# Kernel tuning notes

Hardware: AMD Instinct MI355X
Metric: run time of the kernel (lower is better)

The kernel has to match this reference:

```python
import jax, jax.numpy as jnp
import numpy as np

N_NODES = 50000
N_EDGES = 800000
N_GRAPHS = 512
IN_CH, HID_CH, OUT_CH, N_CLASSES = 128, 64, 64, 10


def gcn_conv(x, src, dst, ew, W, b, n_nodes):
    """PyG GCNConv: add self-loops (weight 1), symmetric normalization, x @ W, scatter-add at dst, + bias."""
    xw = x @ W  # [N, out]
    loop = jnp.arange(n_nodes, dtype=src.dtype)
    src_f = jnp.concatenate([src, loop])
    dst_f = jnp.concatenate([dst, loop])
    ew_f = jnp.concatenate([ew, jnp.ones((n_nodes,), dtype=ew.dtype)])
    deg = jax.ops.segment_sum(ew_f, dst_f, num_segments=n_nodes)  # [N]
    dinv = jnp.where(deg > 0, jax.lax.rsqrt(deg), 0.0)
    norm = dinv[src_f] * ew_f * dinv[dst_f]  # [E+N]
    msg = norm[:, None] * xw[src_f]  # gather + scale
    out = jax.ops.segment_sum(msg, dst_f, num_segments=n_nodes)  # scatter-add
    return out + b


def setup_inputs() -> dict:
    key = jax.random.key(0)
    ks = jax.random.split(key, 12)
    x = jax.random.normal(ks[0], (N_NODES, IN_CH), dtype=jnp.float32)
    edge_index = jax.random.randint(ks[1], (2, N_EDGES), 0, N_NODES, dtype=jnp.int64)
    edge_attr = jax.random.uniform(ks[2], (N_EDGES,), dtype=jnp.float32)
    batch = jnp.sort(jax.random.randint(ks[3], (N_NODES,), 0, N_GRAPHS, dtype=jnp.int64))
    def glorot(k, shape):
        lim = np.sqrt(6.0 / (shape[0] + shape[1]))
        return jax.random.uniform(k, shape, jnp.float32, -lim, lim)
    W1 = glorot(ks[4], (IN_CH, HID_CH))
    b1 = jnp.zeros((HID_CH,), jnp.float32)
    W2 = glorot(ks[5], (HID_CH, OUT_CH))
    b2 = jnp.zeros((OUT_CH,), jnp.float32)
    LW1 = glorot(ks[6], (OUT_CH, 32))
    Lb1 = jnp.zeros((32,), jnp.float32)
    LW2 = glorot(ks[7], (32, N_CLASSES))
    Lb2 = jnp.zeros((N_CLASSES,), jnp.float32)
    return {"x": x, "edge_index": edge_index, "edge_attr": edge_attr, "batch": batch,
            "W1": W1, "b1": b1, "W2": W2, "b2": b2,
            "LW1": LW1, "Lb1": Lb1, "LW2": LW2, "Lb2": Lb2}


def reference(x, edge_index, edge_attr, batch, W1, b1, W2, b2, LW1, Lb1, LW2, Lb2):
    src, dst = edge_index[0], edge_index[1]
    h = gcn_conv(x, src, dst, edge_attr, W1, b1, N_NODES)
    h = jax.nn.relu(h)
    h = gcn_conv(h, src, dst, edge_attr, W2, b2, N_NODES)
    # global mean pool over graphs
    sums = jax.ops.segment_sum(h, batch, num_segments=N_GRAPHS)  # [G, OUT]
    cnt = jax.ops.segment_sum(jnp.ones((N_NODES,), h.dtype), batch, num_segments=N_GRAPHS)
    pooled = sums / jnp.maximum(cnt, 1.0)[:, None]
    # head (dropout treated as identity for deterministic reference)
    h1 = pooled @ LW1 + Lb1
    return h1 @ LW2 + Lb2
```

## Files before the change

kernel.cpp:

```cpp
#include <hip/hip_runtime.h>
#include <hip/hip_bf16.h>

static constexpr int NN = 50000;
static constexpr int NE = 800000;
static constexpr int NG = 512;
static constexpr int NB = 196;
static constexpr int GEMM_BLOCKS = (NN + 63) / 64;
static constexpr int HB = 128;

__device__ __forceinline__ float bfu(ushort u) {
    return __uint_as_float((unsigned)u << 16);
}
__device__ __forceinline__ ushort fbf(float f) {
    return __hip_bfloat16_raw(__float2bfloat16(f)).x;
}


__global__ void zero_kernel(float* __restrict__ p, int n) {
    int i = blockIdx.x * blockDim.x + threadIdx.x;
    if (i < n) p[i] = 0.f;
}

template <int K, bool BF16IN>
__device__ __forceinline__ void gemm_body(const void* __restrict__ Xv,
                                          const float* __restrict__ W,
                                          ushort* __restrict__ out,
                                          int row0, float Xs[][68], float Ws[][64]) {
    int tx = threadIdx.x & 15, ty = threadIdx.x >> 4;
    float acc[4][4] = {};
    for (int kb = 0; kb < K; kb += 64) {
        __syncthreads();
        for (int i = threadIdx.x; i < 1024; i += 256) {
            int kk = i >> 4, c4 = i & 15;
            *(float4*)&Ws[kk][c4 * 4] = *(const float4*)&W[(kb + kk) * 64 + c4 * 4];
        }
        if constexpr (BF16IN) {
            const ushort* X = (const ushort*)Xv;
            for (int i = threadIdx.x; i < 512; i += 256) {
                int r = i >> 3, g = i & 7;
                int gr = row0 + r; if (gr >= NN) gr = NN - 1;
                uint4 v = *(const uint4*)(X + (long long)gr * K + kb + g * 8);
                float4 f0, f1;
                f0.x = __uint_as_float(v.x << 16); f0.y = __uint_as_float(v.x & 0xffff0000u);
                f0.z = __uint_as_float(v.y << 16); f0.w = __uint_as_float(v.y & 0xffff0000u);
                f1.x = __uint_as_float(v.z << 16); f1.y = __uint_as_float(v.z & 0xffff0000u);
                f1.z = __uint_as_float(v.w << 16); f1.w = __uint_as_float(v.w & 0xffff0000u);
                *(float4*)&Xs[r][g * 8] = f0;
                *(float4*)&Xs[r][g * 8 + 4] = f1;
            }
        } else {
            const float* X = (const float*)Xv;
            for (int i = threadIdx.x; i < 1024; i += 256) {
                int r = i >> 4, k4 = i & 15;
                int gr = row0 + r; if (gr >= NN) gr = NN - 1;
                float4 v = *(const float4*)(X + (long long)gr * K + kb + k4 * 4);
                *(float4*)&Xs[r][k4 * 4] = v;
            }
        }
        __syncthreads();
#pragma unroll
        for (int k4 = 0; k4 < 16; ++k4) {
            float4 w0 = *(const float4*)&Ws[k4 * 4 + 0][tx * 4];
            float4 w1 = *(const float4*)&Ws[k4 * 4 + 1][tx * 4];
            float4 w2 = *(const float4*)&Ws[k4 * 4 + 2][tx * 4];
            float4 w3 = *(const float4*)&Ws[k4 * 4 + 3][tx * 4];
            float4 x0 = *(const float4*)&Xs[ty * 4 + 0][k4 * 4];
            float4 x1 = *(const float4*)&Xs[ty * 4 + 1][k4 * 4];
            float4 x2 = *(const float4*)&Xs[ty * 4 + 2][k4 * 4];
            float4 x3 = *(const float4*)&Xs[ty * 4 + 3][k4 * 4];
#define GCN_ROW(j, xv) \
            acc[j][0]=fmaf(xv.x,w0.x,acc[j][0]); acc[j][1]=fmaf(xv.x,w0.y,acc[j][1]); \
            acc[j][2]=fmaf(xv.x,w0.z,acc[j][2]); acc[j][3]=fmaf(xv.x,w0.w,acc[j][3]); \
            acc[j][0]=fmaf(xv.y,w1.x,acc[j][0]); acc[j][1]=fmaf(xv.y,w1.y,acc[j][1]); \
            acc[j][2]=fmaf(xv.y,w1.z,acc[j][2]); acc[j][3]=fmaf(xv.y,w1.w,acc[j][3]); \
            acc[j][0]=fmaf(xv.z,w2.x,acc[j][0]); acc[j][1]=fmaf(xv.z,w2.y,acc[j][1]); \
            acc[j][2]=fmaf(xv.z,w2.z,acc[j][2]); acc[j][3]=fmaf(xv.z,w2.w,acc[j][3]); \
            acc[j][0]=fmaf(xv.w,w3.x,acc[j][0]); acc[j][1]=fmaf(xv.w,w3.y,acc[j][1]); \
            acc[j][2]=fmaf(xv.w,w3.z,acc[j][2]); acc[j][3]=fmaf(xv.w,w3.w,acc[j][3]);
            GCN_ROW(0, x0)
            GCN_ROW(1, x1)
            GCN_ROW(2, x2)
            GCN_ROW(3, x3)
#undef GCN_ROW
        }
    }
#pragma unroll
    for (int j = 0; j < 4; ++j) {
        int r = row0 + ty * 4 + j;
        if (r < NN) {
            ushort4 sv;
            sv.x = fbf(acc[j][0]); sv.y = fbf(acc[j][1]);
            sv.z = fbf(acc[j][2]); sv.w = fbf(acc[j][3]);
            *(ushort4*)(out + (long long)r * 64 + tx * 4) = sv;
        }
    }
}

__global__ __launch_bounds__(256) void hist_gemm_kernel(const int* __restrict__ dst,
                                                        const float* __restrict__ ew,
                                                        unsigned long long* __restrict__ h,
                                                        int* __restrict__ rank,
                                                        const float* __restrict__ X,
                                                        const float* __restrict__ W,
                                                        ushort* __restrict__ out) {
    __shared__ float Xs[64][68];
    __shared__ float Ws[64][64];
    if (blockIdx.x < HB) {
        for (int e = blockIdx.x * 256 + threadIdx.x; e < NE; e += HB * 256) {
            int d = dst[e];
            unsigned int fx = __float2uint_rn(ew[e] * 1048576.0f);
            unsigned long long pack = (1ULL << 40) | (unsigned long long)fx;
            unsigned long long old = atomicAdd(&h[d], pack);
            rank[e] = (int)(old >> 40);
        }
        return;
    }
    gemm_body<128, false>(X, W, out, (blockIdx.x - HB) * 64, Xs, Ws);
}

template <int K, bool BF16IN>
__global__ __launch_bounds__(256) void gemm_kernel(const void* __restrict__ Xv,
                                                   const float* __restrict__ W,
                                                   ushort* __restrict__ out) {
    __shared__ float Xs[64][68];
    __shared__ float Ws[64][64];
    gemm_body<K, BF16IN>(Xv, W, out, blockIdx.x * 64, Xs, Ws);
}

__global__ __launch_bounds__(256) void dinv_scanA_kernel(const unsigned long long* __restrict__ h,
                                                         float* __restrict__ dinv,
                                                         int* __restrict__ partial) {
    int i = blockIdx.x * 256 + threadIdx.x;
    int cnt = 0;
    if (i < NN) {
        unsigned long long v = h[i];
        cnt = (int)(v >> 40);
        float deg = (float)(v & ((1ULL << 40) - 1)) * (1.0f / 1048576.0f) + 1.0f;
        dinv[i] = 1.0f / sqrtf(deg);
    }
    __shared__ int wsum[4];
    int lane = threadIdx.x & 63, wid = threadIdx.x >> 6;
    int v = cnt;
#pragma unroll
    for (int off = 32; off > 0; off >>= 1) v += __shfl_down(v, (unsigned)off, 64);
    if (lane == 0) wsum[wid] = v;
    __syncthreads();
    if (threadIdx.x == 0) partial[blockIdx.x] = wsum[0] + wsum[1] + wsum[2] + wsum[3];
}

__device__ __forceinline__ int block_scan_inclusive(int v, int* wtot) {
    int lane = threadIdx.x & 63, wid = threadIdx.x >> 6;
    int inc = v;
#pragma unroll
    for (int off = 1; off < 64; off <<= 1) {
        int n = __shfl_up(inc, (unsigned)off, 64);
        if (lane >= off) inc += n;
    }
    if (lane == 63) wtot[wid] = inc;
    __syncthreads();
    int add = 0;
    for (int w = 0; w < wid; ++w) add += wtot[w];
    return inc + add;
}

__global__ __launch_bounds__(256) void scanC_bounds_kernel(const unsigned long long* __restrict__ h,
                                                           const int* __restrict__ partial,
                                                           int* __restrict__ rowptr,
                                                           const int* __restrict__ batch,
                                                           int* __restrict__ gbeg,
                                                           int* __restrict__ gend) {
    __shared__ int wtot[4];
    __shared__ int poff_s;
    int t = threadIdx.x;
    if (t < 64) {
        int s = 0;
        for (int i = t; i < (int)blockIdx.x; i += 64) s += partial[i];
#pragma unroll
        for (int off = 32; off > 0; off >>= 1) s += __shfl_down(s, (unsigned)off, 64);
        if (t == 0) poff_s = s;
    }
    int i = blockIdx.x * 256 + t;
    int v = (i < NN) ? (int)(h[i] >> 40) : 0;
    int incl = block_scan_inclusive(v, wtot);
    if (i < NN) {
        rowptr[i + 1] = poff_s + incl;
        int g = batch[i];
        if (i == 0 || batch[i - 1] != g) gbeg[g] = i;
        if (i == NN - 1 || batch[i + 1] != g) gend[g] = i + 1;
    }
    if (i == 0) rowptr[0] = 0;
}

__global__ __launch_bounds__(256) void scatter_kernel(const int* __restrict__ src,
                                                      const int* __restrict__ dst,
                                                      const float* __restrict__ ew,
                                                      const float* __restrict__ dinv,
                                                      const int* __restrict__ rowptr,
                                                      const int* __restrict__ rank,
                                                      int2* __restrict__ epack) {
    int e = blockIdx.x * blockDim.x + threadIdx.x;
    if (e >= NE) return;
    int s = src[e], d = dst[e];
    int pos = rowptr[d] + rank[e];
    float coef = dinv[s] * ew[e];
    epack[pos] = make_int2(s, __float_as_int(coef));
}

template <bool RELU>
__global__ __launch_bounds__(256) void agg_kernel(const ushort* __restrict__ xw,
                                                  const int* __restrict__ rowptr,
                                                  const int2* __restrict__ epack,
                                                  const float* __restrict__ dinv,
                                                  const float* __restrict__ bias,
                                                  ushort* __restrict__ out) {
    int node = blockIdx.x * 4 + (threadIdx.x >> 6);
    if (node >= NN) return;
    int lane = threadIdx.x & 63;
    int q = lane >> 4;
    int l = lane & 15;
    int beg = rowptr[node], end = rowptr[node + 1];
    float a0 = 0.f, a1 = 0.f, a2 = 0.f, a3 = 0.f;
    float b0 = 0.f, b1 = 0.f, b2 = 0.f, b3 = 0.f;
    int j = beg + q;
    for (; j + 4 < end; j += 8) {
        int2 pA = epack[j];
        int2 pB = epack[j + 4];
        ushort4 uA = *(const ushort4*)(xw + pA.x * 64 + 4 * l);
        ushort4 uB = *(const ushort4*)(xw + pB.x * 64 + 4 * l);
        float wA = __int_as_float(pA.y);
        float wB = __int_as_float(pB.y);
        a0 = fmaf(wA, bfu(uA.x), a0); a1 = fmaf(wA, bfu(uA.y), a1);
        a2 = fmaf(wA, bfu(uA.z), a2); a3 = fmaf(wA, bfu(uA.w), a3);
        b0 = fmaf(wB, bfu(uB.x), b0); b1 = fmaf(wB, bfu(uB.y), b1);
        b2 = fmaf(wB, bfu(uB.z), b2); b3 = fmaf(wB, bfu(uB.w), b3);
    }
    if (j < end) {
        int2 pA = epack[j];
        ushort4 uA = *(const ushort4*)(xw + pA.x * 64 + 4 * l);
        float wA = __int_as_float(pA.y);
        a0 = fmaf(wA, bfu(uA.x), a0); a1 = fmaf(wA, bfu(uA.y), a1);
        a2 = fmaf(wA, bfu(uA.z), a2); a3 = fmaf(wA, bfu(uA.w), a3);
    }
    a0 += b0; a1 += b1; a2 += b2; a3 += b3;
    a0 += __shfl_xor(a0, 16); a0 += __shfl_xor(a0, 32);
    a1 += __shfl_xor(a1, 16); a1 += __shfl_xor(a1, 32);
    a2 += __shfl_xor(a2, 16); a2 += __shfl_xor(a2, 32);
    a3 += __shfl_xor(a3, 16); a3 += __shfl_xor(a3, 32);
    if (q == 0) {
        float di = dinv[node];
        float d2 = di * di;
        ushort4 us = *(const ushort4*)(xw + node * 64 + 4 * l);
        float4 bv = *(const float4*)(bias + 4 * l);
        float o0 = fmaf(di, a0, fmaf(d2, bfu(us.x), bv.x));
        float o1 = fmaf(di, a1, fmaf(d2, bfu(us.y), bv.y));
        float o2 = fmaf(di, a2, fmaf(d2, bfu(us.z), bv.z));
        float o3 = fmaf(di, a3, fmaf(d2, bfu(us.w), bv.w));
        if (RELU) {
            o0 = fmaxf(o0, 0.f); o1 = fmaxf(o1, 0.f);
            o2 = fmaxf(o2, 0.f); o3 = fmaxf(o3, 0.f);
        }
        ushort4 sv;
        sv.x = fbf(o0); sv.y = fbf(o1); sv.z = fbf(o2); sv.w = fbf(o3);
        *(ushort4*)(out + node * 64 + 4 * l) = sv;
    }
}

__global__ __launch_bounds__(256) void poolhead_kernel(const ushort* __restrict__ h,
                                                       const int* __restrict__ gbeg,
                                                       const int* __restrict__ gend,
                                                       const float* __restrict__ LW1,
                                                       const float* __restrict__ Lb1,
                                                       const float* __restrict__ LW2,
                                                       const float* __restrict__ Lb2,
                                                       float* __restrict__ out) {
    __shared__ float pp[4][64];
    __shared__ float p[64];
    __shared__ float t1[32];
    int g = blockIdx.x, t = threadIdx.x;
    int lane = t & 63, wid = t >> 6;
    int b = gbeg[g], e = gend[g];
    float acc = 0.f;
    for (int i = b + wid; i < e; i += 4) acc += bfu(h[i * 64 + lane]);
    pp[wid][lane] = acc;
    __syncthreads();
    if (t < 64) {
        float s = pp[0][t] + pp[1][t] + pp[2][t] + pp[3][t];
        p[t] = s / fmaxf((float)(e - b), 1.0f);
    }
    __syncthreads();
    if (t < 32) {
        float a = Lb1[t];
#pragma unroll
        for (int k = 0; k < 64; ++k) a = fmaf(p[k], LW1[k * 32 + t], a);
        t1[t] = a;
    }
    __syncthreads();
    if (t < 10) {
        float a = Lb2[t];
#pragma unroll
        for (int j = 0; j < 32; ++j) a = fmaf(t1[j], LW2[j * 10 + t], a);
        out[g * 10 + t] = a;
    }
}


extern "C" void kernel_launch(void* const* d_in, const int* in_sizes, int n_in,
                              void* d_out, int out_size, void* d_ws, size_t ws_size,
                              hipStream_t stream) {
    const float* x     = (const float*)d_in[0];
    const int*   ei    = (const int*)d_in[1];
    const float* ew    = (const float*)d_in[2];
    const int*   batch = (const int*)d_in[3];
    const float* W1    = (const float*)d_in[4];
    const float* b1    = (const float*)d_in[5];
    const float* W2    = (const float*)d_in[6];
    const float* b2    = (const float*)d_in[7];
    const float* LW1   = (const float*)d_in[8];
    const float* Lb1   = (const float*)d_in[9];
    const float* LW2   = (const float*)d_in[10];
    const float* Lb2   = (const float*)d_in[11];

    const int* src = ei;
    const int* dst = ei + NE;

    float* ws = (float*)d_ws;
    unsigned long long* h64 = (unsigned long long*)ws;
    int*   gbeg   = (int*)(ws + 100096);
    int*   gend   = (int*)(ws + 100608);
    float* dinv   = ws + 101120;
    int*   rowptr = (int*)(ws + 151168);
    int*   partial= (int*)(ws + 201216);
    int2*  epack  = (int2*)(ws + 201472);
    ushort* xwA   = (ushort*)(ws + 1801472);
    ushort* h12   = (ushort*)(ws + 3401472);
    int*   rank   = (int*)(ws + 5001472);

    zero_kernel<<<(101120 + 255) / 256, 256, 0, stream>>>(ws, 101120);

    hist_gemm_kernel<<<HB + GEMM_BLOCKS, 256, 0, stream>>>(dst, ew, h64, rank, x, W1, xwA);
    dinv_scanA_kernel<<<NB, 256, 0, stream>>>(h64, dinv, partial);
    scanC_bounds_kernel<<<NB, 256, 0, stream>>>(h64, partial, rowptr, batch, gbeg, gend);
    scatter_kernel<<<(NE + 255) / 256, 256, 0, stream>>>(src, dst, ew, dinv, rowptr, rank, epack);

    agg_kernel<true><<<(NN + 3) / 4, 256, 0, stream>>>(xwA, rowptr, epack, dinv, b1, h12);

    gemm_kernel<64, true><<<GEMM_BLOCKS, 256, 0, stream>>>(h12, W2, xwA);
    agg_kernel<false><<<(NN + 3) / 4, 256, 0, stream>>>(xwA, rowptr, epack, dinv, b2, h12);

    poolhead_kernel<<<NG, 256, 0, stream>>>(h12, gbeg, gend, LW1, Lb1, LW2, Lb2, (float*)d_out);
}
```

Baseline: 243.7 us.

## Split degree histogram into two tables, merge scan kernels, widen aggregation loads

The degree/rank histogram now alternates edges between two atomic tables by thread parity to halve contention, with more histogram blocks and two atomics issued per loop iteration; scatter adds the first table's count for odd edges. The two scan passes are merged into one kernel that recomputes block prefix offsets directly from the histograms and also computes dinv, removing a launch. The aggregation kernel now processes 8 edges per wave with 16-byte row loads and 8 accumulators. Costs include zeroing a larger workspace and redundant prefix summation in each scan block.

```diff
diff --git a/kernel.cpp b/kernel.cpp
--- a/kernel.cpp
+++ b/kernel.cpp
@@ -6,7 +6,7 @@
 static constexpr int NG = 512;
 static constexpr int NB = 196;
 static constexpr int GEMM_BLOCKS = (NN + 63) / 64;
-static constexpr int HB = 128;
+static constexpr int HB = 240;
 
 __device__ __forceinline__ float bfu(ushort u) {
     return __uint_as_float((unsigned)u << 16);
@@ -98,7 +98,8 @@
 
 __global__ __launch_bounds__(256) void hist_gemm_kernel(const int* __restrict__ dst,
                                                         const float* __restrict__ ew,
-                                                        unsigned long long* __restrict__ h,
+                                                        unsigned long long* __restrict__ hA,
+                                                        unsigned long long* __restrict__ hB,
                                                         int* __restrict__ rank,
                                                         const float* __restrict__ X,
                                                         const float* __restrict__ W,
@@ -106,12 +107,25 @@
     __shared__ float Xs[64][68];
     __shared__ float Ws[64][64];
     if (blockIdx.x < HB) {
-        for (int e = blockIdx.x * 256 + threadIdx.x; e < NE; e += HB * 256) {
-            int d = dst[e];
-            unsigned int fx = __float2uint_rn(ew[e] * 1048576.0f);
-            unsigned long long pack = (1ULL << 40) | (unsigned long long)fx;
-            unsigned long long old = atomicAdd(&h[d], pack);
-            rank[e] = (int)(old >> 40);
+        const int T = HB * 256;
+        int tid = blockIdx.x * 256 + threadIdx.x;
+        unsigned long long* tab = (tid & 1) ? hB : hA;
+        for (int e = tid; e < NE; e += 2 * T) {
+            int e1 = e + T;
+            bool has1 = e1 < NE;
+            int d0 = dst[e];
+            float v0 = ew[e];
+            int d1 = has1 ? dst[e1] : 0;
+            float v1 = has1 ? ew[e1] : 0.f;
+            unsigned long long p0 = (1ULL << 40) |
+                (unsigned long long)__float2uint_rn(v0 * 1048576.0f);
+            unsigned long long p1 = (1ULL << 40) |
+                (unsigned long long)__float2uint_rn(v1 * 1048576.0f);
+            unsigned long long o0 = atomicAdd(&tab[d0], p0);
+            unsigned long long o1 = 0;
+            if (has1) o1 = atomicAdd(&tab[d1], p1);
+            rank[e] = (int)(o0 >> 40);
+            if (has1) rank[e1] = (int)(o1 >> 40);
         }
         return;
     }
@@ -127,27 +141,6 @@
     gemm_body<K, BF16IN>(Xv, W, out, blockIdx.x * 64, Xs, Ws);
 }
 
-__global__ __launch_bounds__(256) void dinv_scanA_kernel(const unsigned long long* __restrict__ h,
-                                                         float* __restrict__ dinv,
-                                                         int* __restrict__ partial) {
-    int i = blockIdx.x * 256 + threadIdx.x;
-    int cnt = 0;
-    if (i < NN) {
-        unsigned long long v = h[i];
-        cnt = (int)(v >> 40);
-        float deg = (float)(v & ((1ULL << 40) - 1)) * (1.0f / 1048576.0f) + 1.0f;
-        dinv[i] = 1.0f / sqrtf(deg);
-    }
-    __shared__ int wsum[4];
-    int lane = threadIdx.x & 63, wid = threadIdx.x >> 6;
-    int v = cnt;
-#pragma unroll
-    for (int off = 32; off > 0; off >>= 1) v += __shfl_down(v, (unsigned)off, 64);
-    if (lane == 0) wsum[wid] = v;
-    __syncthreads();
-    if (threadIdx.x == 0) partial[blockIdx.x] = wsum[0] + wsum[1] + wsum[2] + wsum[3];
-}
-
 __device__ __forceinline__ int block_scan_inclusive(int v, int* wtot) {
     int lane = threadIdx.x & 63, wid = threadIdx.x >> 6;
     int inc = v;
@@ -163,27 +156,38 @@
     return inc + add;
 }
 
-__global__ __launch_bounds__(256) void scanC_bounds_kernel(const unsigned long long* __restrict__ h,
-                                                           const int* __restrict__ partial,
-                                                           int* __restrict__ rowptr,
-                                                           const int* __restrict__ batch,
-                                                           int* __restrict__ gbeg,
-                                                           int* __restrict__ gend) {
+__global__ __launch_bounds__(256) void scan_kernel(const unsigned long long* __restrict__ hA,
+                                                   const unsigned long long* __restrict__ hB,
+                                                   float* __restrict__ dinv,
+                                                   int* __restrict__ rowptr,
+                                                   const int* __restrict__ batch,
+                                                   int* __restrict__ gbeg,
+                                                   int* __restrict__ gend) {
+    __shared__ int ws4[4];
     __shared__ int wtot[4];
-    __shared__ int poff_s;
     int t = threadIdx.x;
-    if (t < 64) {
-        int s = 0;
-        for (int i = t; i < (int)blockIdx.x; i += 64) s += partial[i];
-#pragma unroll
-        for (int off = 32; off > 0; off >>= 1) s += __shfl_down(s, (unsigned)off, 64);
-        if (t == 0) poff_s = s;
-    }
-    int i = blockIdx.x * 256 + t;
-    int v = (i < NN) ? (int)(h[i] >> 40) : 0;
-    int incl = block_scan_inclusive(v, wtot);
+    int start = blockIdx.x * 256;
+    int s = 0;
+    for (int j = t; j < start; j += 256)
+        s += (int)(hA[j] >> 40) + (int)(hB[j] >> 40);
+    int lane = t & 63, wid = t >> 6;
+#pragma unroll
+    for (int off = 32; off > 0; off >>= 1) s += __shfl_down(s, (unsigned)off, 64);
+    if (lane == 0) ws4[wid] = s;
+    __syncthreads();
+    int poff = ws4[0] + ws4[1] + ws4[2] + ws4[3];
+    int i = start + t;
+    int cnt = 0;
     if (i < NN) {
-        rowptr[i + 1] = poff_s + incl;
+        unsigned long long va = hA[i], vb = hB[i];
+        constexpr unsigned long long M = (1ULL << 40) - 1;
+        cnt = (int)(va >> 40) + (int)(vb >> 40);
+        float deg = (float)((va & M) + (vb & M)) * (1.0f / 1048576.0f) + 1.0f;
+        dinv[i] = 1.0f / sqrtf(deg);
+    }
+    int incl = block_scan_inclusive(cnt, wtot);
+    if (i < NN) {
+        rowptr[i + 1] = poff + incl;
         int g = batch[i];
         if (i == 0 || batch[i - 1] != g) gbeg[g] = i;
         if (i == NN - 1 || batch[i + 1] != g) gend[g] = i + 1;
@@ -197,11 +201,13 @@
                                                       const float* __restrict__ dinv,
                                                       const int* __restrict__ rowptr,
                                                       const int* __restrict__ rank,
+                                                      const unsigned long long* __restrict__ hA,
                                                       int2* __restrict__ epack) {
     int e = blockIdx.x * blockDim.x + threadIdx.x;
     if (e >= NE) return;
     int s = src[e], d = dst[e];
     int pos = rowptr[d] + rank[e];
+    if (e & 1) pos += (int)(hA[d] >> 40);
     float coef = dinv[s] * ew[e];
     epack[pos] = make_int2(s, __float_as_int(coef));
 }
@@ -216,52 +222,51 @@
     int node = blockIdx.x * 4 + (threadIdx.x >> 6);
     if (node >= NN) return;
     int lane = threadIdx.x & 63;
-    int q = lane >> 4;
-    int l = lane & 15;
+    int e8 = lane >> 3;
+    int l8 = lane & 7;
     int beg = rowptr[node], end = rowptr[node + 1];
     float a0 = 0.f, a1 = 0.f, a2 = 0.f, a3 = 0.f;
-    float b0 = 0.f, b1 = 0.f, b2 = 0.f, b3 = 0.f;
-    int j = beg + q;
-    for (; j + 4 < end; j += 8) {
-        int2 pA = epack[j];
-        int2 pB = epack[j + 4];
-        ushort4 uA = *(const ushort4*)(xw + pA.x * 64 + 4 * l);
-        ushort4 uB = *(const ushort4*)(xw + pB.x * 64 + 4 * l);
-        float wA = __int_as_float(pA.y);
-        float wB = __int_as_float(pB.y);
-        a0 = fmaf(wA, bfu(uA.x), a0); a1 = fmaf(wA, bfu(uA.y), a1);
-        a2 = fmaf(wA, bfu(uA.z), a2); a3 = fmaf(wA, bfu(uA.w), a3);
-        b0 = fmaf(wB, bfu(uB.x), b0); b1 = fmaf(wB, bfu(uB.y), b1);
-        b2 = fmaf(wB, bfu(uB.z), b2); b3 = fmaf(wB, bfu(uB.w), b3);
-    }
-    if (j < end) {
-        int2 pA = epack[j];
-        ushort4 uA = *(const ushort4*)(xw + pA.x * 64 + 4 * l);
-        float wA = __int_as_float(pA.y);
-        a0 = fmaf(wA, bfu(uA.x), a0); a1 = fmaf(wA, bfu(uA.y), a1);
-        a2 = fmaf(wA, bfu(uA.z), a2); a3 = fmaf(wA, bfu(uA.w), a3);
-    }
-    a0 += b0; a1 += b1; a2 += b2; a3 += b3;
-    a0 += __shfl_xor(a0, 16); a0 += __shfl_xor(a0, 32);
-    a1 += __shfl_xor(a1, 16); a1 += __shfl_xor(a1, 32);
-    a2 += __shfl_xor(a2, 16); a2 += __shfl_xor(a2, 32);
-    a3 += __shfl_xor(a3, 16); a3 += __shfl_xor(a3, 32);
-    if (q == 0) {
+    float a4 = 0.f, a5 = 0.f, a6 = 0.f, a7 = 0.f;
+    for (int j = beg + e8; j < end; j += 8) {
+        int2 p = epack[j];
+        uint4 v = *(const uint4*)(xw + p.x * 64 + l8 * 8);
+        float w = __int_as_float(p.y);
+        a0 = fmaf(w, __uint_as_float(v.x << 16), a0);
+        a1 = fmaf(w, __uint_as_float(v.x & 0xffff0000u), a1);
+        a2 = fmaf(w, __uint_as_float(v.y << 16), a2);
+        a3 = fmaf(w, __uint_as_float(v.y & 0xffff0000u), a3);
+        a4 = fmaf(w, __uint_as_float(v.z << 16), a4);
+        a5 = fmaf(w, __uint_as_float(v.z & 0xffff0000u), a5);
+        a6 = fmaf(w, __uint_as_float(v.w << 16), a6);
+        a7 = fmaf(w, __uint_as_float(v.w & 0xffff0000u), a7);
+    }
+#define RED(x) x += __shfl_xor(x, 8); x += __shfl_xor(x, 16); x += __shfl_xor(x, 32);
+    RED(a0) RED(a1) RED(a2) RED(a3) RED(a4) RED(a5) RED(a6) RED(a7)
+#undef RED
+    if (e8 == 0) {
         float di = dinv[node];
         float d2 = di * di;
-        ushort4 us = *(const ushort4*)(xw + node * 64 + 4 * l);
-        float4 bv = *(const float4*)(bias + 4 * l);
-        float o0 = fmaf(di, a0, fmaf(d2, bfu(us.x), bv.x));
-        float o1 = fmaf(di, a1, fmaf(d2, bfu(us.y), bv.y));
-        float o2 = fmaf(di, a2, fmaf(d2, bfu(us.z), bv.z));
-        float o3 = fmaf(di, a3, fmaf(d2, bfu(us.w), bv.w));
+        uint4 us = *(const uint4*)(xw + node * 64 + l8 * 8);
+        float4 bv0 = *(const float4*)(bias + l8 * 8);
+        float4 bv1 = *(const float4*)(bias + l8 * 8 + 4);
+        float o0 = fmaf(di, a0, fmaf(d2, __uint_as_float(us.x << 16), bv0.x));
+        float o1 = fmaf(di, a1, fmaf(d2, __uint_as_float(us.x & 0xffff0000u), bv0.y));
+        float o2 = fmaf(di, a2, fmaf(d2, __uint_as_float(us.y << 16), bv0.z));
+        float o3 = fmaf(di, a3, fmaf(d2, __uint_as_float(us.y & 0xffff0000u), bv0.w));
+        float o4 = fmaf(di, a4, fmaf(d2, __uint_as_float(us.z << 16), bv1.x));
+        float o5 = fmaf(di, a5, fmaf(d2, __uint_as_float(us.z & 0xffff0000u), bv1.y));
+        float o6 = fmaf(di, a6, fmaf(d2, __uint_as_float(us.w << 16), bv1.z));
+        float o7 = fmaf(di, a7, fmaf(d2, __uint_as_float(us.w & 0xffff0000u), bv1.w));
         if (RELU) {
-            o0 = fmaxf(o0, 0.f); o1 = fmaxf(o1, 0.f);
-            o2 = fmaxf(o2, 0.f); o3 = fmaxf(o3, 0.f);
-        }
-        ushort4 sv;
-        sv.x = fbf(o0); sv.y = fbf(o1); sv.z = fbf(o2); sv.w = fbf(o3);
-        *(ushort4*)(out + node * 64 + 4 * l) = sv;
+            o0 = fmaxf(o0, 0.f); o1 = fmaxf(o1, 0.f); o2 = fmaxf(o2, 0.f); o3 = fmaxf(o3, 0.f);
+            o4 = fmaxf(o4, 0.f); o5 = fmaxf(o5, 0.f); o6 = fmaxf(o6, 0.f); o7 = fmaxf(o7, 0.f);
+        }
+        uint4 sv;
+        sv.x = (unsigned)fbf(o0) | ((unsigned)fbf(o1) << 16);
+        sv.y = (unsigned)fbf(o2) | ((unsigned)fbf(o3) << 16);
+        sv.z = (unsigned)fbf(o4) | ((unsigned)fbf(o5) << 16);
+        sv.w = (unsigned)fbf(o6) | ((unsigned)fbf(o7) << 16);
+        *(uint4*)(out + node * 64 + l8 * 8) = sv;
     }
 }
 
@@ -324,23 +329,24 @@
     const int* dst = ei + NE;
 
     float* ws = (float*)d_ws;
-    unsigned long long* h64 = (unsigned long long*)ws;
-    int*   gbeg   = (int*)(ws + 100096);
-    int*   gend   = (int*)(ws + 100608);
-    float* dinv   = ws + 101120;
-    int*   rowptr = (int*)(ws + 151168);
-    int*   partial= (int*)(ws + 201216);
-    int2*  epack  = (int2*)(ws + 201472);
-    ushort* xwA   = (ushort*)(ws + 1801472);
-    ushort* h12   = (ushort*)(ws + 3401472);
-    int*   rank   = (int*)(ws + 5001472);
-
-    zero_kernel<<<(101120 + 255) / 256, 256, 0, stream>>>(ws, 101120);
-
-    hist_gemm_kernel<<<HB + GEMM_BLOCKS, 256, 0, stream>>>(dst, ew, h64, rank, x, W1, xwA);
-    dinv_scanA_kernel<<<NB, 256, 0, stream>>>(h64, dinv, partial);
-    scanC_bounds_kernel<<<NB, 256, 0, stream>>>(h64, partial, rowptr, batch, gbeg, gend);
-    scatter_kernel<<<(NE + 255) / 256, 256, 0, stream>>>(src, dst, ew, dinv, rowptr, rank, epack);
+    unsigned long long* hA = (unsigned long long*)ws;
+    unsigned long long* hB = (unsigned long long*)(ws + 100096);
+    int*   gbeg   = (int*)(ws + 200192);
+    int*   gend   = (int*)(ws + 200704);
+    float* dinv   = ws + 201216;
+    int*   rowptr = (int*)(ws + 251264);
+    int2*  epack  = (int2*)(ws + 301312);
+    ushort* xwA   = (ushort*)(ws + 1901312);
+    ushort* h12   = (ushort*)(ws + 3501312);
+    int*   rank   = (int*)(ws + 5101312);
+
+    zero_kernel<<<(201216 + 255) / 256, 256, 0, stream>>>(ws, 201216);
+
+    hist_gemm_kernel<<<HB + GEMM_BLOCKS, 256, 0, stream>>>(dst, ew, hA, hB, rank,
+                                                           x, W1, xwA);
+    scan_kernel<<<NB, 256, 0, stream>>>(hA, hB, dinv, rowptr, batch, gbeg, gend);
+    scatter_kernel<<<(NE + 255) / 256, 256, 0, stream>>>(src, dst, ew, dinv, rowptr,
+                                                         rank, hA, epack);
 
     agg_kernel<true><<<(NN + 3) / 4, 256, 0, stream>>>(xwA, rowptr, epack, dinv, b1, h12);
 
```

New measurement: 303.2 us. 24.4% more time.
